# Optimization experiments

Hardware: AMD Instinct MI355X
Metric: run time of the kernel (lower is better)

The kernel has to match this reference:

```python
import jax, jax.numpy as jnp
import numpy as np

EPS = 1e-5

@jax.custom_vjp
def round_ste(x):
    return jnp.round(x)

def _round_fwd(x):
    return jnp.round(x), None

def _round_bwd(_, g):
    return (g,)

round_ste.defvjp(_round_fwd, _round_bwd)


def setup_inputs() -> dict:
    key = jax.random.key(0)
    ks = jax.random.split(key, 4)
    x = jax.random.normal(ks[0], (16, 64, 128, 128), dtype=jnp.float32)
    # small init so conv outputs stay in a sane range
    W = jax.random.normal(ks[1], (128, 64, 3, 3), dtype=jnp.float32) * 0.05
    gamma = jnp.ones((128,), dtype=jnp.float32)
    beta = jnp.zeros((128,), dtype=jnp.float32)
    mean = jax.random.normal(ks[2], (128,), dtype=jnp.float32) * 0.1
    var = jax.random.uniform(ks[3], (128,), dtype=jnp.float32) * 0.5 + 0.5
    # Brevitas QuantReLU default learned max ~6.0 (relu6-like init)
    act_scale = jnp.ones((1,), dtype=jnp.float32) * 6.0
    return {"x": x, "W": W, "gamma": gamma, "beta": beta,
            "mean": mean, "var": var, "act_scale": act_scale}


def reference(x, W, gamma, beta, mean, var, act_scale):
    # --- Int8 per-tensor weight quant-dequant (symmetric, scale = maxabs/127) ---
    w_scale = jnp.max(jnp.abs(W)) / 127.0
    qW = jnp.clip(round_ste(W / w_scale), -127.0, 127.0) * w_scale
    # --- conv2d, stride 1, padding 1, no bias (NCHW / OIHW) ---
    y = jax.lax.conv_general_dilated(
        x, qW, window_strides=(1, 1), padding=[(1, 1), (1, 1)],
        dimension_numbers=("NCHW", "OIHW", "NCHW"))
    # --- BatchNorm (inference form with running stats) ---
    scale = (gamma / jnp.sqrt(var + EPS))[None, :, None, None]
    shift = (beta - gamma * mean / jnp.sqrt(var + EPS))[None, :, None, None]
    y = y * scale + shift
    # --- QuantReLU: relu + uint8 per-tensor quant-dequant ---
    y = jax.nn.relu(y)
    s = act_scale[0] / 255.0
    return jnp.clip(round_ste(y / s), 0.0, 255.0) * s
```

## Files before the change

kernel.cpp:

```cpp
#include <hip/hip_runtime.h>
#include <math.h>

typedef __bf16 bf16x8 __attribute__((ext_vector_type(8)));
typedef float  f32x16 __attribute__((ext_vector_type(16)));

#define CIN    64
#define KOUT   128
#define HGT    128
#define WID    128
#define NBATCH 16
#define BN_EPS 1e-5f

#define WQ_OFF   256u
#define XT_OFF   (1u << 20)
#define WS_NEED  ((size_t)XT_OFF + (size_t)NBATCH * HGT * WID * CIN * 2)

__global__ __launch_bounds__(256) void wmax_kernel(const float* __restrict__ W,
                                                   unsigned* __restrict__ wsmax) {
    int idx = blockIdx.x * 256 + threadIdx.x;
    const float4* W4 = (const float4*)W;
    float4 v = W4[idx];
    float m = fmaxf(fmaxf(fabsf(v.x), fabsf(v.y)), fmaxf(fabsf(v.z), fabsf(v.w)));
    #pragma unroll
    for (int off = 32; off > 0; off >>= 1)
        m = fmaxf(m, __shfl_xor(m, off));
    __shared__ float red[4];
    if ((threadIdx.x & 63) == 0) red[threadIdx.x >> 6] = m;
    __syncthreads();
    if (threadIdx.x == 0) {
        m = fmaxf(fmaxf(red[0], red[1]), fmaxf(red[2], red[3]));
        atomicMax(wsmax, __float_as_uint(m));
    }
}

__global__ __launch_bounds__(256) void pack_w(const float* __restrict__ W,
                                              const unsigned* __restrict__ wsmax,
                                              __bf16* __restrict__ wqp) {
    int bid = blockIdx.x;
    int tap = bid % 9, cs = bid / 9;
    int t = threadIdx.x;
    int lane = t & 63, mf = t >> 6;
    float ws = __uint_as_float(*wsmax) / 127.0f;
    int kout  = mf * 32 + (lane & 31);
    int cbase = cs * 16 + (lane >> 5) * 8;
    bf16x8 o;
    #pragma unroll
    for (int j = 0; j < 8; ++j) {
        float w = W[(size_t)(kout * 64 + cbase + j) * 9 + tap];
        float q = rintf(w / ws);
        q = fminf(fmaxf(q, -127.f), 127.f);
        o[j] = (__bf16)q;
    }
    *(bf16x8*)(wqp + (((size_t)bid * 4 + mf) * 64 + lane) * 8) = o;
}

__global__ __launch_bounds__(256) void xform(const float* __restrict__ x,
                                             __bf16* __restrict__ xT) {
    __shared__ float t[CIN * 32];
    int bid = blockIdx.x;
    int wt = bid & 3;
    int h  = (bid >> 2) & 127;
    int n  = bid >> 9;
    int w0 = wt * 32;
    int tid = threadIdx.x;
    const float* src = x + ((size_t)n * CIN * HGT + h) * WID + w0;
    int wlane = tid & 31;
    int cbase = tid >> 5;
    #pragma unroll
    for (int it = 0; it < 8; ++it) {
        int c = cbase + it * 8;
        t[c * 32 + (wlane ^ (c & 31))] = src[(size_t)c * HGT * WID + wlane];
    }
    __syncthreads();
    int w = tid >> 3;
    int chunk = tid & 7;
    bf16x8 o;
    #pragma unroll
    for (int j = 0; j < 8; ++j) {
        int c = chunk * 8 + j;
        o[j] = (__bf16)t[c * 32 + (w ^ (c & 31))];
    }
    *(bf16x8*)(xT + (((size_t)n * HGT + h) * WID + w0 + w) * CIN + chunk * 8) = o;
}

__global__ __launch_bounds__(256, 2) void conv_mfma(
    const __bf16* __restrict__ xT, const __bf16* __restrict__ wqp,
    const float* __restrict__ gamma, const float* __restrict__ beta,
    const float* __restrict__ mean, const float* __restrict__ var,
    const float* __restrict__ act_scale, const unsigned* __restrict__ wsmax,
    float* __restrict__ out)
{
    __shared__ uint4 xs[2720];
    __shared__ float sc2[KOUT], sh2[KOUT];

    const int bid = blockIdx.x;
    const int wb = bid & 3, hb = (bid >> 2) & 15, n = bid >> 6;
    const int h0 = hb * 8, w0 = wb * 32;
    const int tid  = threadIdx.x;
    const int lane = tid & 63;
    const int wave = tid >> 6;
    const int wm = wave & 1;
    const int wr = wave >> 1;

    const float s_act = act_scale[0] / 255.0f;
    if (tid < KOUT) {
        float ws  = __uint_as_float(*wsmax) / 127.0f;
        float isd = 1.0f / sqrtf(var[tid] + BN_EPS);
        float sc  = ws * gamma[tid] * isd;
        float sh  = beta[tid] - gamma[tid] * mean[tid] * isd;
        sc2[tid] = sc / s_act;
        sh2[tid] = sh / s_act;
    }

    const __bf16* xn = xT + (size_t)n * HGT * WID * CIN;
    for (int it = tid; it < 2720; it += 256) {
        int pl = it >> 3, chunk = it & 7;
        int r = pl / 34, cc = pl - r * 34;
        int gh = h0 - 1 + r, gw = w0 - 1 + cc;
        uint4 v = make_uint4(0u, 0u, 0u, 0u);
        if ((unsigned)gh < HGT && (unsigned)gw < WID)
            v = *(const uint4*)(xn + ((size_t)gh * WID + gw) * CIN + chunk * 8);
        xs[pl * 8 + (chunk ^ (pl & 7))] = v;
    }
    __syncthreads();

    const int nn = lane & 31;
    const int kh = lane >> 5;

    f32x16 acc[2][4];
    #pragma unroll
    for (int a = 0; a < 2; ++a)
        #pragma unroll
        for (int b = 0; b < 4; ++b)
            #pragma unroll
            for (int r = 0; r < 16; ++r) acc[a][b][r] = 0.0f;

    const __bf16* wbase = wqp + ((size_t)(wm * 2) * 64 + lane) * 8;
    #define AFRAG(cs, tap, mf) (*(const bf16x8*)(wbase + (((size_t)(cs) * 9 + (tap)) * 2048) + (size_t)(mf) * 512))

    bf16x8 A[2][2][3];
    #pragma unroll
    for (int dy = 0; dy < 3; ++dy) {
        A[0][0][dy] = AFRAG(0, dy * 3, 0);
        A[0][1][dy] = AFRAG(0, dy * 3, 1);
    }

    #pragma unroll
    for (int it = 0; it < 12; ++it) {
        const int cs = it / 3, dx = it % 3;
        const int cur = it & 1, nxt = cur ^ 1;
        if (it < 11) {
            const int cs2 = (it + 1) / 3, dx2 = (it + 1) % 3;
            #pragma unroll
            for (int dy = 0; dy < 3; ++dy) {
                A[nxt][0][dy] = AFRAG(cs2, dy * 3 + dx2, 0);
                A[nxt][1][dy] = AFRAG(cs2, dy * 3 + dx2, 1);
            }
        }
        const int chb = cs * 2 + kh;
        bf16x8 B[6];
        #pragma unroll
        for (int rr = 0; rr < 6; ++rr) {
            const int pl = (wr * 4 + rr) * 34 + nn + dx;
            B[rr] = *(const bf16x8*)&xs[pl * 8 + (chb ^ (pl & 7))];
        }
        #pragma unroll
        for (int dy = 0; dy < 3; ++dy) {
            #pragma unroll
            for (int nf = 0; nf < 4; ++nf) {
                acc[0][nf] = __builtin_amdgcn_mfma_f32_32x32x16_bf16(A[cur][0][dy], B[nf + dy], acc[0][nf], 0, 0, 0);
                acc[1][nf] = __builtin_amdgcn_mfma_f32_32x32x16_bf16(A[cur][1][dy], B[nf + dy], acc[1][nf], 0, 0, 0);
            }
        }
    }
    #undef AFRAG

    const int wpix = w0 + nn;
    #pragma unroll
    for (int mf = 0; mf < 2; ++mf) {
        #pragma unroll
        for (int nf = 0; nf < 4; ++nf) {
            const int hpix = h0 + wr * 4 + nf;
            #pragma unroll
            for (int reg = 0; reg < 16; ++reg) {
                int k = wm * 64 + mf * 32 + 4 * kh + (reg & 3) + 8 * (reg >> 2);
                float t = fmaf(acc[mf][nf][reg], sc2[k], sh2[k]);
                t = fmaxf(t, 0.0f);
                float q = fminf(rintf(t), 255.0f);
                out[(((size_t)n * KOUT + k) * HGT + hpix) * WID + wpix] = q * s_act;
            }
        }
    }
}

#define CB 4
#define TH 8
#define KB 8
__global__ __launch_bounds__(256) void conv_fallback(
    const float* __restrict__ x, const float* __restrict__ W,
    const float* __restrict__ gamma, const float* __restrict__ beta,
    const float* __restrict__ mean, const float* __restrict__ var,
    const float* __restrict__ act_scale, const unsigned* __restrict__ wsmax,
    float* __restrict__ out)
{
    __shared__ float xsf[CB][TH + 2][WID + 2];
    __shared__ float wsh[CB][9][KB];
    const int bid = blockIdx.x;
    const int hg = bid & 15, kg = (bid >> 4) & 15, n = bid >> 8;
    const int h0 = hg * TH, k0 = kg * KB;
    const int tid = threadIdx.x;
    const int tx = tid & 31, ty = tid >> 5;
    float acc[4][KB];
    #pragma unroll
    for (int j = 0; j < 4; ++j)
        #pragma unroll
        for (int kk = 0; kk < KB; ++kk) acc[j][kk] = 0.f;
    const float w_scale = __uint_as_float(*wsmax) / 127.0f;
    const float* xn = x + (size_t)n * CIN * HGT * WID;
    for (int c0 = 0; c0 < CIN; c0 += CB) {
        __syncthreads();
        for (int i = tid; i < CB * (TH + 2) * (WID + 2); i += 256) {
            int cc = i / ((TH + 2) * (WID + 2));
            int r  = i - cc * ((TH + 2) * (WID + 2));
            int yy = r / (WID + 2);
            int xx = r - yy * (WID + 2);
            int gh = h0 - 1 + yy, gw = xx - 1;
            float v = 0.f;
            if ((unsigned)gh < HGT && (unsigned)gw < WID)
                v = xn[(size_t)(c0 + cc) * HGT * WID + gh * WID + gw];
            xsf[cc][yy][xx] = v;
        }
        for (int i = tid; i < CB * 9 * KB; i += 256) {
            int cc = i / (9 * KB);
            int r  = i - cc * (9 * KB);
            int tap = r / KB, kk = r - tap * KB;
            float w = W[(size_t)((k0 + kk) * CIN + (c0 + cc)) * 9 + tap];
            float q = rintf(w / w_scale);
            q = fminf(fmaxf(q, -127.f), 127.f);
            wsh[cc][tap][kk] = q * w_scale;
        }
        __syncthreads();
        #pragma unroll
        for (int cc = 0; cc < CB; ++cc)
            #pragma unroll
            for (int dy = 0; dy < 3; ++dy) {
                float w0a[KB], w1a[KB], w2a[KB];
                #pragma unroll
                for (int kk = 0; kk < KB; ++kk) {
                    w0a[kk] = wsh[cc][dy * 3 + 0][kk];
                    w1a[kk] = wsh[cc][dy * 3 + 1][kk];
                    w2a[kk] = wsh[cc][dy * 3 + 2][kk];
                }
                const float* row = &xsf[cc][ty + dy][0];
                #pragma unroll
                for (int j = 0; j < 4; ++j) {
                    float v0 = row[tx + 32 * j + 0];
                    float v1 = row[tx + 32 * j + 1];
                    float v2 = row[tx + 32 * j + 2];
                    #pragma unroll
                    for (int kk = 0; kk < KB; ++kk) {
                        acc[j][kk] = fmaf(v0, w0a[kk], acc[j][kk]);
                        acc[j][kk] = fmaf(v1, w1a[kk], acc[j][kk]);
                        acc[j][kk] = fmaf(v2, w2a[kk], acc[j][kk]);
                    }
                }
            }
    }
    const float s_act = act_scale[0] / 255.0f;
    const float inv_s = 1.0f / s_act;
    const int h = h0 + ty;
    #pragma unroll
    for (int kk = 0; kk < KB; ++kk) {
        int k = k0 + kk;
        float isd = 1.0f / sqrtf(var[k] + BN_EPS);
        float sc = gamma[k] * isd;
        float sh = beta[k] - gamma[k] * mean[k] * isd;
        float* orow = out + (((size_t)n * KOUT + k) * HGT + h) * WID;
        #pragma unroll
        for (int j = 0; j < 4; ++j) {
            float y = fmaf(acc[j][kk], sc, sh);
            y = fmaxf(y, 0.f);
            float q = rintf(y * inv_s);
            q = fminf(q, 255.f);
            orow[tx + 32 * j] = q * s_act;
        }
    }
}

extern "C" void kernel_launch(void* const* d_in, const int* in_sizes, int n_in,
                              void* d_out, int out_size, void* d_ws, size_t ws_size,
                              hipStream_t stream) {
    const float* x         = (const float*)d_in[0];
    const float* W         = (const float*)d_in[1];
    const float* gamma     = (const float*)d_in[2];
    const float* beta      = (const float*)d_in[3];
    const float* mean      = (const float*)d_in[4];
    const float* var       = (const float*)d_in[5];
    const float* act_scale = (const float*)d_in[6];
    unsigned* wsmax = (unsigned*)d_ws;

    hipMemsetAsync(d_ws, 0, sizeof(unsigned), stream);
    wmax_kernel<<<72, 256, 0, stream>>>(W, wsmax);

    if (ws_size >= WS_NEED) {
        __bf16* wqp = (__bf16*)((char*)d_ws + WQ_OFF);
        __bf16* xT  = (__bf16*)((char*)d_ws + XT_OFF);
        pack_w<<<36, 256, 0, stream>>>(W, wsmax, wqp);
        xform<<<NBATCH * HGT * 4, 256, 0, stream>>>(x, xT);
        conv_mfma<<<NBATCH * 64, 256, 0, stream>>>(
            xT, wqp, gamma, beta, mean, var, act_scale, wsmax, (float*)d_out);
    } else {
        conv_fallback<<<4096, 256, 0, stream>>>(
            x, W, gamma, beta, mean, var, act_scale, wsmax, (float*)d_out);
    }
}
```

Before: 86.24 us.

## Split conv output channels across 8 waves with 512-thread blocks

Raises the conv block to 512 threads (8 waves) so each wave owns one 32-channel M-fragment instead of two. This halves accumulator registers per wave and drops the A-fragment double-buffer prefetch, aiming for higher occupancy via launch_bounds(512,4). Each B fragment is now read from LDS by twice as many waves, and weight loads are no longer prefetched ahead of the MFMAs, which could expose global load latency.

```diff
diff --git a/kernel.cpp b/kernel.cpp
--- a/kernel.cpp
+++ b/kernel.cpp
@@ -83,7 +83,7 @@
     *(bf16x8*)(xT + (((size_t)n * HGT + h) * WID + w0 + w) * CIN + chunk * 8) = o;
 }
 
-__global__ __launch_bounds__(256, 2) void conv_mfma(
+__global__ __launch_bounds__(512, 4) void conv_mfma(
     const __bf16* __restrict__ xT, const __bf16* __restrict__ wqp,
     const float* __restrict__ gamma, const float* __restrict__ beta,
     const float* __restrict__ mean, const float* __restrict__ var,
@@ -99,8 +99,8 @@
     const int tid  = threadIdx.x;
     const int lane = tid & 63;
     const int wave = tid >> 6;
-    const int wm = wave & 1;
-    const int wr = wave >> 1;
+    const int wmf = wave & 3;
+    const int wr  = wave >> 2;
 
     const float s_act = act_scale[0] / 255.0f;
     if (tid < KOUT) {
@@ -113,7 +113,7 @@
     }
 
     const __bf16* xn = xT + (size_t)n * HGT * WID * CIN;
-    for (int it = tid; it < 2720; it += 256) {
+    for (int it = tid; it < 2720; it += 512) {
         int pl = it >> 3, chunk = it & 7;
         int r = pl / 34, cc = pl - r * 34;
         int gh = h0 - 1 + r, gw = w0 - 1 + cc;
@@ -127,36 +127,22 @@
     const int nn = lane & 31;
     const int kh = lane >> 5;
 
-    f32x16 acc[2][4];
-    #pragma unroll
-    for (int a = 0; a < 2; ++a)
-        #pragma unroll
-        for (int b = 0; b < 4; ++b)
-            #pragma unroll
-            for (int r = 0; r < 16; ++r) acc[a][b][r] = 0.0f;
-
-    const __bf16* wbase = wqp + ((size_t)(wm * 2) * 64 + lane) * 8;
-    #define AFRAG(cs, tap, mf) (*(const bf16x8*)(wbase + (((size_t)(cs) * 9 + (tap)) * 2048) + (size_t)(mf) * 512))
-
-    bf16x8 A[2][2][3];
-    #pragma unroll
-    for (int dy = 0; dy < 3; ++dy) {
-        A[0][0][dy] = AFRAG(0, dy * 3, 0);
-        A[0][1][dy] = AFRAG(0, dy * 3, 1);
-    }
+    f32x16 acc[4];
+    #pragma unroll
+    for (int b = 0; b < 4; ++b)
+        #pragma unroll
+        for (int r = 0; r < 16; ++r) acc[b][r] = 0.0f;
+
+    const __bf16* wbase = wqp + ((size_t)wmf * 64 + lane) * 8;
+    #define AFRAG(cs, tap) (*(const bf16x8*)(wbase + ((size_t)((cs) * 9 + (tap)) * 2048)))
 
     #pragma unroll
     for (int it = 0; it < 12; ++it) {
         const int cs = it / 3, dx = it % 3;
-        const int cur = it & 1, nxt = cur ^ 1;
-        if (it < 11) {
-            const int cs2 = (it + 1) / 3, dx2 = (it + 1) % 3;
-            #pragma unroll
-            for (int dy = 0; dy < 3; ++dy) {
-                A[nxt][0][dy] = AFRAG(cs2, dy * 3 + dx2, 0);
-                A[nxt][1][dy] = AFRAG(cs2, dy * 3 + dx2, 1);
-            }
-        }
+        bf16x8 A[3];
+        #pragma unroll
+        for (int dy = 0; dy < 3; ++dy)
+            A[dy] = AFRAG(cs, dy * 3 + dx);
         const int chb = cs * 2 + kh;
         bf16x8 B[6];
         #pragma unroll
@@ -168,8 +154,7 @@
         for (int dy = 0; dy < 3; ++dy) {
             #pragma unroll
             for (int nf = 0; nf < 4; ++nf) {
-                acc[0][nf] = __builtin_amdgcn_mfma_f32_32x32x16_bf16(A[cur][0][dy], B[nf + dy], acc[0][nf], 0, 0, 0);
-                acc[1][nf] = __builtin_amdgcn_mfma_f32_32x32x16_bf16(A[cur][1][dy], B[nf + dy], acc[1][nf], 0, 0, 0);
+                acc[nf] = __builtin_amdgcn_mfma_f32_32x32x16_bf16(A[dy], B[nf + dy], acc[nf], 0, 0, 0);
             }
         }
     }
@@ -177,18 +162,15 @@
 
     const int wpix = w0 + nn;
     #pragma unroll
-    for (int mf = 0; mf < 2; ++mf) {
-        #pragma unroll
-        for (int nf = 0; nf < 4; ++nf) {
-            const int hpix = h0 + wr * 4 + nf;
-            #pragma unroll
-            for (int reg = 0; reg < 16; ++reg) {
-                int k = wm * 64 + mf * 32 + 4 * kh + (reg & 3) + 8 * (reg >> 2);
-                float t = fmaf(acc[mf][nf][reg], sc2[k], sh2[k]);
-                t = fmaxf(t, 0.0f);
-                float q = fminf(rintf(t), 255.0f);
-                out[(((size_t)n * KOUT + k) * HGT + hpix) * WID + wpix] = q * s_act;
-            }
+    for (int nf = 0; nf < 4; ++nf) {
+        const int hpix = h0 + wr * 4 + nf;
+        #pragma unroll
+        for (int reg = 0; reg < 16; ++reg) {
+            int k = wmf * 32 + 4 * kh + (reg & 3) + 8 * (reg >> 2);
+            float t = fmaf(acc[nf][reg], sc2[k], sh2[k]);
+            t = fmaxf(t, 0.0f);
+            float q = fminf(rintf(t), 255.0f);
+            out[(((size_t)n * KOUT + k) * HGT + hpix) * WID + wpix] = q * s_act;
         }
     }
 }
@@ -307,7 +289,7 @@
         __bf16* xT  = (__bf16*)((char*)d_ws + XT_OFF);
         pack_w<<<36, 256, 0, stream>>>(W, wsmax, wqp);
         xform<<<NBATCH * HGT * 4, 256, 0, stream>>>(x, xT);
-        conv_mfma<<<NBATCH * 64, 256, 0, stream>>>(
+        conv_mfma<<<NBATCH * 64, 512, 0, stream>>>(
             xT, wqp, gamma, beta, mean, var, act_scale, wsmax, (float*)d_out);
     } else {
         conv_fallback<<<4096, 256, 0, stream>>>(
```

Result: slower. 101.2 us (+17.4%).
